# Optimization experiments

Hardware: AMD Instinct MI355X
Metric: run time of the kernel (lower is better)

The kernel has to match this reference:

```python
import jax, jax.numpy as jnp
import numpy as np

TAU = 0.5

def setup_inputs() -> dict:
    key = jax.random.key(0)
    ks = jax.random.split(key, 8)
    B_Nq, B_Ns, C, H, W = 16, 16, 512, 32, 32
    f_q = jax.random.normal(ks[0], (B_Nq, C, H, W), dtype=jnp.float32)
    f_s = jax.random.normal(ks[1], (B_Ns, C, H, W), dtype=jnp.float32)
    # depthwise 1x1 convs with groups=dim, bias=False -> per-channel scalar weights [C]
    w_cca_q = jax.random.normal(ks[2], (C,), dtype=jnp.float32)
    w_cca_k = jax.random.normal(ks[3], (C,), dtype=jnp.float32)
    w_cca_v = jax.random.normal(ks[4], (C,), dtype=jnp.float32)
    w_sca_q = jax.random.normal(ks[5], (C,), dtype=jnp.float32)
    w_sca_k = jax.random.normal(ks[6], (C,), dtype=jnp.float32)
    lam = jnp.float32(0.1)
    return {"f_q": f_q, "f_s": f_s, "w_cca_q": w_cca_q, "w_cca_k": w_cca_k,
            "w_cca_v": w_cca_v, "w_sca_q": w_sca_q, "w_sca_k": w_sca_k, "lam": lam}

def _dw(x, w):
    # depthwise 1x1 conv, no bias == per-channel scale; x: [B,C,H,W], w: [C]
    return x * w[None, :, None, None]

def reference(f_q, f_s, w_cca_q, w_cca_k, w_cca_v, w_sca_q, w_sca_k, lam):
    B_Nq, C, H, W = f_q.shape
    B_Ns = f_s.shape[0]
    P = H * W
    qc = _dw(f_q, w_cca_q).reshape(B_Nq, C, P)          # [B,C,P]
    kc_mean = _dw(f_s, w_cca_k).reshape(B_Ns, C, P).mean(axis=0)  # [C,P]
    vc_mean = _dw(f_s, w_cca_v).reshape(B_Ns, C, P).mean(axis=0)  # [C,P]
    # channel attention: [B,C,C]
    Ac = jax.nn.softmax(jnp.einsum('bcp,dp->bcd', qc, kc_mean) / P, axis=-1)
    f_cca_q = jnp.einsum('bcd,dp->bcp', Ac, vc_mean).reshape(B_Nq, C, H, W)
    qs = _dw(f_cca_q, w_sca_q).reshape(B_Nq, C, P)      # [B,C,P]
    ks_mean = _dw(f_s, w_sca_k).reshape(B_Ns, C, P).mean(axis=0)  # [C,P]
    # spatial affinity: [B,P,P]
    M = jnp.einsum('bcp,cq->bpq', qs, ks_mean) / (TAU * C)
    alpha = jax.nn.softmax(M.mean(axis=-1), axis=-1)    # [B_Nq,P]
    beta = jax.nn.softmax(M.mean(axis=-2), axis=-1)     # [B_Nq,P]
    beta_mean = jnp.broadcast_to(beta.mean(axis=0, keepdims=True), (B_Ns, P))
    Fq_out = f_q + lam * f_cca_q
    return (Fq_out, alpha, beta_mean)
```

## Files before the change

### kernel.cpp

```cpp
#include <hip/hip_runtime.h>

typedef __bf16 bf16;
typedef __bf16 bf16x4 __attribute__((ext_vector_type(4)));
typedef __bf16 bf16x8 __attribute__((ext_vector_type(8)));
typedef float f32x4 __attribute__((ext_vector_type(4)));


#define GLL16(g, l)                                                             \
    __builtin_amdgcn_global_load_lds((const __attribute__((address_space(1))) void*)(g), \
                                     (__attribute__((address_space(3))) void*)(l), 16, 0, 0)

__device__ inline float wave_reduce_sum(float v) {
#pragma unroll
    for (int m = 32; m >= 1; m >>= 1) v += __shfl_xor(v, m, 64);
    return v;
}
__device__ inline float wave_reduce_max(float v) {
#pragma unroll
    for (int m = 32; m >= 1; m >>= 1) v = fmaxf(v, __shfl_xor(v, m, 64));
    return v;
}

__global__ void k_prep(const float* __restrict__ fs, const float* __restrict__ fq,
                       float* __restrict__ fsm32, bf16* __restrict__ fsm16,
                       bf16* __restrict__ fsmT, bf16* __restrict__ fq16,
                       float* __restrict__ rmpart) {
    __shared__ bf16 tile[32][33];
    int bx = blockIdx.x, by = blockIdx.y;
    int p0 = bx * 32, c0 = by * 32;
    int t = threadIdx.x;
    int cy = t >> 3, px = (t & 7) * 4;
    size_t off = (size_t)(c0 + cy) * 1024 + p0 + px;
    float4 s = {0.f, 0.f, 0.f, 0.f};
#pragma unroll
    for (int b = 0; b < 16; ++b) {
        float4 v = *(const float4*)(fs + (size_t)b * 524288 + off);
        s.x += v.x; s.y += v.y; s.z += v.z; s.w += v.w;
    }
    s.x *= (1.f / 16.f); s.y *= (1.f / 16.f); s.z *= (1.f / 16.f); s.w *= (1.f / 16.f);
    *(float4*)(fsm32 + off) = s;
    bf16x4 h4 = {(bf16)s.x, (bf16)s.y, (bf16)s.z, (bf16)s.w};
    *(bf16x4*)(fsm16 + off) = h4;
    tile[cy][px] = h4[0];
    tile[cy][px + 1] = h4[1];
    tile[cy][px + 2] = h4[2];
    tile[cy][px + 3] = h4[3];
    float rp = s.x + s.y + s.z + s.w;
    rp += __shfl_xor(rp, 1, 64);
    rp += __shfl_xor(rp, 2, 64);
    rp += __shfl_xor(rp, 4, 64);
    if ((t & 7) == 0) rmpart[bx * 512 + c0 + cy] = rp;
    __syncthreads();
    int tx = t & 31, ty = t >> 5;
#pragma unroll
    for (int i = 0; i < 4; ++i)
        fsmT[(size_t)(p0 + ty + 8 * i) * 512 + c0 + tx] = tile[tx][ty + 8 * i];
    int blk = by * 32 + bx;
    const float4* f4 = (const float4*)fq;
#pragma unroll
    for (int i = 0; i < 16; ++i) {
        int idx = blk * 4096 + i * 256 + t;
        float4 v = f4[idx];
        bf16x4 q4 = {(bf16)v.x, (bf16)v.y, (bf16)v.z, (bf16)v.w};
        *(bf16x4*)(fq16 + (size_t)idx * 4) = q4;
    }
}

__global__ void k_gemm1(const bf16* __restrict__ A, const bf16* __restrict__ B,
                        const float* __restrict__ rmpart, const float* __restrict__ wsq,
                        const float* __restrict__ wsk, float* __restrict__ rm,
                        float* __restrict__ u, float* __restrict__ G) {
    __shared__ alignas(16) bf16 As[2][64 * 64];
    __shared__ alignas(16) bf16 Bs[2][128 * 64];
    const int dt = blockIdx.x, ct = blockIdx.y, b = blockIdx.z;
    const int t = threadIdx.x, w = t >> 6, lane = t & 63;
    const int quad = lane >> 4, r15 = lane & 15;
    const int wr = w & 1, wc = w >> 1;
    if (dt == 0 && b == 0) {
        int c = ct * 64 + (t >> 2);
        float sum = 0.f;
#pragma unroll
        for (int j = 0; j < 8; ++j) sum += rmpart[((t & 3) * 8 + j) * 512 + c];
        sum += __shfl_xor(sum, 1, 64);
        sum += __shfl_xor(sum, 2, 64);
        if ((t & 3) == 0) {
            float rmv = sum * (1.f / 1024.f);
            rm[c] = rmv;
            u[c] = wsq[c] * wsk[c] * rmv * (1.f / 256.f);
        }
    }
    const bf16* Abase = A + ((size_t)(b * 512 + ct * 64)) * 1024;
    const bf16* Bbase = B + ((size_t)(dt * 128)) * 1024;
    f32x4 acc[2][4] = {};
    auto STAGE = [&](int buf, int k0) {
#pragma unroll
        for (int i = 0; i < 2; ++i) {
            int row = i * 32 + (t >> 3);
            int gchunk = (t & 7) ^ (row & 7);
            GLL16(Abase + (size_t)row * 1024 + k0 + gchunk * 8, &As[buf][(i * 256 + t) * 8]);
        }
#pragma unroll
        for (int i = 0; i < 4; ++i) {
            int row = i * 32 + (t >> 3);
            int gchunk = (t & 7) ^ (row & 7);
            GLL16(Bbase + (size_t)row * 1024 + k0 + gchunk * 8, &Bs[buf][(i * 256 + t) * 8]);
        }
    };
    STAGE(0, 0);
    STAGE(1, 64);
    for (int s = 0; s < 16; ++s) {
        if (s < 15) asm volatile("s_waitcnt vmcnt(6)" ::: "memory");
        else        asm volatile("s_waitcnt vmcnt(0)" ::: "memory");
        __builtin_amdgcn_s_barrier();
        const int cur = s & 1;
#pragma unroll
        for (int ks = 0; ks < 2; ++ks) {
            bf16x8 af[2], bfr[4];
            const int c8 = ks * 4 + quad;
#pragma unroll
            for (int mi = 0; mi < 2; ++mi) {
                int R = wr * 32 + mi * 16 + r15;
                af[mi] = *(const bf16x8*)(&As[cur][R * 64 + ((c8 ^ (R & 7)) * 8)]);
            }
#pragma unroll
            for (int j = 0; j < 4; ++j) {
                int R = wc * 64 + j * 16 + r15;
                bfr[j] = *(const bf16x8*)(&Bs[cur][R * 64 + ((c8 ^ (R & 7)) * 8)]);
            }
#pragma unroll
            for (int mi = 0; mi < 2; ++mi)
#pragma unroll
                for (int j = 0; j < 4; ++j)
                    acc[mi][j] = __builtin_amdgcn_mfma_f32_16x16x32_bf16(af[mi], bfr[j], acc[mi][j], 0, 0, 0);
        }
        __builtin_amdgcn_s_barrier();
        if (s + 2 < 16) STAGE(cur, (s + 2) * 64);
    }
#pragma unroll
    for (int mi = 0; mi < 2; ++mi) {
        float* g = G + ((size_t)(b * 512 + ct * 64 + wr * 32 + mi * 16 + quad * 4)) * 512 +
                   dt * 128 + wc * 64 + r15;
#pragma unroll
        for (int j = 0; j < 4; ++j)
#pragma unroll
            for (int ii = 0; ii < 4; ++ii)
                g[(size_t)ii * 512 + j * 16] = acc[mi][j][ii];
    }
}

__global__ void k_softmax_ac(const float* __restrict__ G, const float* __restrict__ wq,
                             const float* __restrict__ wk, const float* __restrict__ wv,
                             const float* __restrict__ rm, bf16* __restrict__ Acw,
                             float* __restrict__ r, float* __restrict__ zbuf) {
    if (blockIdx.x < 133) zbuf[blockIdx.x * 256 + threadIdx.x] = 0.f;
    int row = blockIdx.x * 4 + (threadIdx.x >> 6);
    int lane = threadIdx.x & 63;
    int c = row & 511;
    const float* g = G + (size_t)row * 512;
    float sc = wq[c] * (1.f / 1024.f);
    float v[8];
    float mx = -3.4e38f;
#pragma unroll
    for (int j = 0; j < 8; ++j) {
        int d = lane + 64 * j;
        v[j] = g[d] * sc * wk[d];
        mx = fmaxf(mx, v[j]);
    }
    mx = wave_reduce_max(mx);
    float sum = 0.f;
#pragma unroll
    for (int j = 0; j < 8; ++j) {
        v[j] = __expf(v[j] - mx);
        sum += v[j];
    }
    sum = wave_reduce_sum(sum);
    float inv = 1.f / sum;
    bf16* o = Acw + (size_t)row * 512;
    float rsum = 0.f;
#pragma unroll
    for (int j = 0; j < 8; ++j) {
        int d = lane + 64 * j;
        float aw = v[j] * inv * wv[d];
        o[d] = (bf16)aw;
        rsum += aw * rm[d];
    }
    rsum = wave_reduce_sum(rsum);
    if (lane == 0) r[row] = rsum;
}

__global__ void k_gemm2(const bf16* __restrict__ A, const bf16* __restrict__ B,
                        const float* __restrict__ fq, const float* __restrict__ lamp,
                        const float* __restrict__ u, const float* __restrict__ r,
                        const float* __restrict__ wsq, const float* __restrict__ wsk,
                        const float* __restrict__ fsm32, float* __restrict__ out,
                        float* __restrict__ alog, float* __restrict__ blog) {
    __shared__ alignas(16) bf16 As[2][64 * 64];
    __shared__ alignas(16) bf16 Bs[2][128 * 64];
    const int pt = blockIdx.x, ct = blockIdx.y, b = blockIdx.z;
    const int t = threadIdx.x, w = t >> 6, lane = t & 63;
    const int quad = lane >> 4, r15 = lane & 15;
    const int wr = w & 1, wc = w >> 1;
    const bf16* Abase = A + ((size_t)(b * 512 + ct * 64)) * 512;
    const bf16* Bbase = B + ((size_t)(pt * 128)) * 512;
    f32x4 acc[2][4] = {};
    auto STAGE = [&](int buf, int k0) {
#pragma unroll
        for (int i = 0; i < 2; ++i) {
            int row = i * 32 + (t >> 3);
            int gchunk = (t & 7) ^ (row & 7);
            GLL16(Abase + (size_t)row * 512 + k0 + gchunk * 8, &As[buf][(i * 256 + t) * 8]);
        }
#pragma unroll
        for (int i = 0; i < 4; ++i) {
            int row = i * 32 + (t >> 3);
            int gchunk = (t & 7) ^ (row & 7);
            GLL16(Bbase + (size_t)row * 512 + k0 + gchunk * 8, &Bs[buf][(i * 256 + t) * 8]);
        }
    };
    STAGE(0, 0);
    STAGE(1, 64);
    for (int s = 0; s < 8; ++s) {
        if (s < 7) asm volatile("s_waitcnt vmcnt(6)" ::: "memory");
        else       asm volatile("s_waitcnt vmcnt(0)" ::: "memory");
        __builtin_amdgcn_s_barrier();
        const int cur = s & 1;
#pragma unroll
        for (int ks = 0; ks < 2; ++ks) {
            bf16x8 af[2], bfr[4];
            const int c8 = ks * 4 + quad;
#pragma unroll
            for (int mi = 0; mi < 2; ++mi) {
                int R = wr * 32 + mi * 16 + r15;
                af[mi] = *(const bf16x8*)(&As[cur][R * 64 + ((c8 ^ (R & 7)) * 8)]);
            }
#pragma unroll
            for (int j = 0; j < 4; ++j) {
                int R = wc * 64 + j * 16 + r15;
                bfr[j] = *(const bf16x8*)(&Bs[cur][R * 64 + ((c8 ^ (R & 7)) * 8)]);
            }
#pragma unroll
            for (int mi = 0; mi < 2; ++mi)
#pragma unroll
                for (int j = 0; j < 4; ++j)
                    acc[mi][j] = __builtin_amdgcn_mfma_f32_16x16x32_bf16(af[mi], bfr[j], acc[mi][j], 0, 0, 0);
        }
        __builtin_amdgcn_s_barrier();
        if (s + 2 < 8) STAGE(cur, (s + 2) * 64);
    }
    float lam = lamp[0];
#pragma unroll
    for (int mi = 0; mi < 2; ++mi) {
        size_t rowbase = (size_t)(b * 512 + ct * 64 + wr * 32 + mi * 16 + quad * 4);
#pragma unroll
        for (int j = 0; j < 4; ++j)
#pragma unroll
            for (int ii = 0; ii < 4; ++ii) {
                size_t idx = (rowbase + ii) * 1024 + pt * 128 + wc * 64 + j * 16 + r15;
                out[idx] = fq[idx] + lam * acc[mi][j][ii];
            }
    }
    float uv[2][4];
#pragma unroll
    for (int mi = 0; mi < 2; ++mi)
#pragma unroll
        for (int ii = 0; ii < 4; ++ii)
            uv[mi][ii] = u[ct * 64 + wr * 32 + mi * 16 + quad * 4 + ii];
#pragma unroll
    for (int j = 0; j < 4; ++j) {
        float pv = 0.f;
#pragma unroll
        for (int mi = 0; mi < 2; ++mi)
#pragma unroll
            for (int ii = 0; ii < 4; ++ii)
                pv += uv[mi][ii] * acc[mi][j][ii];
        pv += __shfl_xor(pv, 16, 64);
        pv += __shfl_xor(pv, 32, 64);
        if (lane < 16)
            atomicAdd(alog + (size_t)b * 1024 + pt * 128 + wc * 64 + j * 16 + r15, pv);
    }
    if (ct == 0) {
        __shared__ float coef[512];
        coef[t] = r[b * 512 + t] * wsq[t] * wsk[t] * (1.f / 256.f);
        coef[t + 256] = r[b * 512 + t + 256] * wsq[t + 256] * wsk[t + 256] * (1.f / 256.f);
        __syncthreads();
        int q = pt * 128 + (t & 127);
        int ch = t >> 7;
        const float* f = fsm32 + (size_t)(ch * 256) * 1024 + q;
        const float* cf = coef + ch * 256;
        float s0 = 0.f, s1 = 0.f, s2 = 0.f, s3 = 0.f;
#pragma unroll 4
        for (int ci = 0; ci < 256; ci += 4) {
            s0 += cf[ci] * f[(size_t)ci * 1024];
            s1 += cf[ci + 1] * f[(size_t)(ci + 1) * 1024];
            s2 += cf[ci + 2] * f[(size_t)(ci + 2) * 1024];
            s3 += cf[ci + 3] * f[(size_t)(ci + 3) * 1024];
        }
        atomicAdd(&blog[(size_t)b * 1024 + q], (s0 + s1) + (s2 + s3));
    }
}

__global__ void k_softmax_rows(const float* __restrict__ alog, const float* __restrict__ blog,
                               float* __restrict__ alpha_out, float* __restrict__ bmean,
                               int* __restrict__ cnt, float* __restrict__ out_bmean) {
    int z = blockIdx.x;
    int t = threadIdx.x;
    int w = t >> 6, lane = t & 63;
    const float* src = (z < 16) ? (alog + (size_t)z * 1024) : (blog + (size_t)(z - 16) * 1024);
    float v[4];
    float mx = -3.4e38f;
#pragma unroll
    for (int j = 0; j < 4; ++j) {
        v[j] = src[t + 256 * j];
        mx = fmaxf(mx, v[j]);
    }
    __shared__ float red[4];
    float wm = wave_reduce_max(mx);
    if (lane == 0) red[w] = wm;
    __syncthreads();
    mx = fmaxf(fmaxf(red[0], red[1]), fmaxf(red[2], red[3]));
    float s = 0.f;
#pragma unroll
    for (int j = 0; j < 4; ++j) {
        v[j] = __expf(v[j] - mx);
        s += v[j];
    }
    __syncthreads();
    float ws_ = wave_reduce_sum(s);
    if (lane == 0) red[w] = ws_;
    __syncthreads();
    s = red[0] + red[1] + red[2] + red[3];
    float inv = 1.f / s;
    if (z < 16) {
#pragma unroll
        for (int j = 0; j < 4; ++j) alpha_out[(size_t)z * 1024 + t + 256 * j] = v[j] * inv;
    } else {
        float inv16 = inv * (1.f / 16.f);
#pragma unroll
        for (int j = 0; j < 4; ++j) atomicAdd(&bmean[t + 256 * j], v[j] * inv16);
        __threadfence();
        __syncthreads();
        __shared__ int lastflag;
        if (t == 0) lastflag = (atomicAdd(cnt, 1) == 15) ? 1 : 0;
        __syncthreads();
        if (lastflag) {
            __threadfence();
#pragma unroll
            for (int j = 0; j < 4; ++j) {
                int q = t + 256 * j;
                float val = __hip_atomic_load(&bmean[q], __ATOMIC_ACQUIRE, __HIP_MEMORY_SCOPE_AGENT);
#pragma unroll
                for (int si = 0; si < 16; ++si) out_bmean[(size_t)si * 1024 + q] = val;
            }
        }
    }
}

extern "C" void kernel_launch(void* const* d_in, const int* in_sizes, int n_in,
                              void* d_out, int out_size, void* d_ws, size_t ws_size,
                              hipStream_t stream) {
    const float* f_q = (const float*)d_in[0];
    const float* f_s = (const float*)d_in[1];
    const float* w_cca_q = (const float*)d_in[2];
    const float* w_cca_k = (const float*)d_in[3];
    const float* w_cca_v = (const float*)d_in[4];
    const float* w_sca_q = (const float*)d_in[5];
    const float* w_sca_k = (const float*)d_in[6];
    const float* lamp = (const float*)d_in[7];

    char* ws = (char*)d_ws;
    float* fsm32 = (float*)(ws + 0);
    bf16* fsm16 = (bf16*)(ws + 2097152);
    bf16* fsmT = (bf16*)(ws + 3145728);
    float* G = (float*)(ws + 4194304);
    bf16* Acw = (bf16*)(ws + 20971520);
    bf16* fq16 = (bf16*)(ws + 29360128);
    float* rmpart = (float*)(ws + 46137344);
    float* rm = (float*)(ws + 46202880);
    float* u = (float*)(ws + 46204928);
    float* r = (float*)(ws + 46206976);
    float* alog = (float*)(ws + 46239744);
    float* blog = (float*)(ws + 46305280);
    float* bmean = (float*)(ws + 46370816);
    int* cnt = (int*)(ws + 46374912);

    float* out_fq = (float*)d_out;
    float* out_alpha = out_fq + 8388608;
    float* out_bmean = out_fq + 8404992;

    k_prep<<<dim3(32, 16), 256, 0, stream>>>(f_s, f_q, fsm32, fsm16, fsmT, fq16, rmpart);
    k_gemm1<<<dim3(4, 8, 16), 256, 0, stream>>>(fq16, fsm16, rmpart, w_sca_q, w_sca_k, rm, u, G);
    k_softmax_ac<<<2048, 256, 0, stream>>>(G, w_cca_q, w_cca_k, w_cca_v, rm, Acw, r, alog);
    k_gemm2<<<dim3(8, 8, 16), 256, 0, stream>>>(Acw, fsmT, f_q, lamp, u, r, w_sca_q, w_sca_k,
                                                fsm32, out_fq, alog, blog);
    k_softmax_rows<<<32, 256, 0, stream>>>(alog, blog, out_alpha, bmean, cnt, out_bmean);
}
```

Baseline: 172.8 us.

## Fuse five kernels into one cooperative persistent kernel with grid syncs

Replaces the five separate launches (prep, gemm1, channel softmax, gemm2, row softmax) with a single cooperative kernel of 512 blocks that runs each stage in turn, separated by grid.sync(). Stages that previously used more blocks now loop over virtual block ids. The aim is to remove per-launch overhead and inter-kernel gaps. In exchange, parallelism is capped at 512 resident blocks, gemm2 runs two tiles per block serially, the last stage uses only 32 blocks while the others idle, and every grid barrier has its own cost.

```diff
diff --git a/kernel.cpp b/kernel.cpp
--- a/kernel.cpp
+++ b/kernel.cpp
@@ -1,4 +1,7 @@
 #include <hip/hip_runtime.h>
+#include <hip/hip_cooperative_groups.h>
+
+namespace cg = cooperative_groups;
 
 typedef __bf16 bf16;
 typedef __bf16 bf16x4 __attribute__((ext_vector_type(4)));
@@ -21,335 +24,355 @@
     return v;
 }
 
-__global__ void k_prep(const float* __restrict__ fs, const float* __restrict__ fq,
-                       float* __restrict__ fsm32, bf16* __restrict__ fsm16,
-                       bf16* __restrict__ fsmT, bf16* __restrict__ fq16,
-                       float* __restrict__ rmpart) {
-    __shared__ bf16 tile[32][33];
-    int bx = blockIdx.x, by = blockIdx.y;
-    int p0 = bx * 32, c0 = by * 32;
-    int t = threadIdx.x;
-    int cy = t >> 3, px = (t & 7) * 4;
-    size_t off = (size_t)(c0 + cy) * 1024 + p0 + px;
-    float4 s = {0.f, 0.f, 0.f, 0.f};
-#pragma unroll
-    for (int b = 0; b < 16; ++b) {
-        float4 v = *(const float4*)(fs + (size_t)b * 524288 + off);
-        s.x += v.x; s.y += v.y; s.z += v.z; s.w += v.w;
+struct KParams {
+    const float* fq;
+    const float* fs;
+    const float* wq;
+    const float* wk;
+    const float* wv;
+    const float* wsq;
+    const float* wsk;
+    const float* lamp;
+    float* fsm32;
+    bf16* fsm16;
+    bf16* fsmT;
+    bf16* fq16;
+    float* rmpart;
+    float* rm;
+    float* u;
+    float* G;
+    bf16* Acw;
+    float* r;
+    float* alog;
+    float* blog;
+    float* bmean;
+    int* cnt;
+    float* out_fq;
+    float* out_alpha;
+    float* out_bmean;
+};
+
+__global__ void __launch_bounds__(256, 2) k_mega(KParams P) {
+    __shared__ __align__(16) char smem[53248];
+    cg::grid_group grid = cg::this_grid();
+    const int bid = blockIdx.x;
+    const int t = threadIdx.x;
+    const int w = t >> 6, lane = t & 63;
+    const int quad = lane >> 4, r15 = lane & 15;
+
+    {
+        bf16(*tile)[33] = (bf16(*)[33])(smem + 49152);
+        int bx = bid & 31, by = bid >> 5;
+        int p0 = bx * 32, c0 = by * 32;
+        int cy = t >> 3, px = (t & 7) * 4;
+        size_t off = (size_t)(c0 + cy) * 1024 + p0 + px;
+        float4 s = {0.f, 0.f, 0.f, 0.f};
+#pragma unroll
+        for (int b = 0; b < 16; ++b) {
+            float4 v = *(const float4*)(P.fs + (size_t)b * 524288 + off);
+            s.x += v.x; s.y += v.y; s.z += v.z; s.w += v.w;
+        }
+        s.x *= (1.f / 16.f); s.y *= (1.f / 16.f); s.z *= (1.f / 16.f); s.w *= (1.f / 16.f);
+        *(float4*)(P.fsm32 + off) = s;
+        bf16x4 h4 = {(bf16)s.x, (bf16)s.y, (bf16)s.z, (bf16)s.w};
+        *(bf16x4*)(P.fsm16 + off) = h4;
+        tile[cy][px] = h4[0];
+        tile[cy][px + 1] = h4[1];
+        tile[cy][px + 2] = h4[2];
+        tile[cy][px + 3] = h4[3];
+        float rp = s.x + s.y + s.z + s.w;
+        rp += __shfl_xor(rp, 1, 64);
+        rp += __shfl_xor(rp, 2, 64);
+        rp += __shfl_xor(rp, 4, 64);
+        if ((t & 7) == 0) P.rmpart[bx * 512 + c0 + cy] = rp;
+        __syncthreads();
+        int tx = t & 31, ty = t >> 5;
+#pragma unroll
+        for (int i = 0; i < 4; ++i)
+            P.fsmT[(size_t)(p0 + ty + 8 * i) * 512 + c0 + tx] = tile[tx][ty + 8 * i];
+        int blk = by * 32 + bx;
+        const float4* f4 = (const float4*)P.fq;
+#pragma unroll
+        for (int i = 0; i < 16; ++i) {
+            int idx = blk * 4096 + i * 256 + t;
+            float4 v = f4[idx];
+            bf16x4 q4 = {(bf16)v.x, (bf16)v.y, (bf16)v.z, (bf16)v.w};
+            *(bf16x4*)(P.fq16 + (size_t)idx * 4) = q4;
+        }
     }
-    s.x *= (1.f / 16.f); s.y *= (1.f / 16.f); s.z *= (1.f / 16.f); s.w *= (1.f / 16.f);
-    *(float4*)(fsm32 + off) = s;
-    bf16x4 h4 = {(bf16)s.x, (bf16)s.y, (bf16)s.z, (bf16)s.w};
-    *(bf16x4*)(fsm16 + off) = h4;
-    tile[cy][px] = h4[0];
-    tile[cy][px + 1] = h4[1];
-    tile[cy][px + 2] = h4[2];
-    tile[cy][px + 3] = h4[3];
-    float rp = s.x + s.y + s.z + s.w;
-    rp += __shfl_xor(rp, 1, 64);
-    rp += __shfl_xor(rp, 2, 64);
-    rp += __shfl_xor(rp, 4, 64);
-    if ((t & 7) == 0) rmpart[bx * 512 + c0 + cy] = rp;
-    __syncthreads();
-    int tx = t & 31, ty = t >> 5;
-#pragma unroll
-    for (int i = 0; i < 4; ++i)
-        fsmT[(size_t)(p0 + ty + 8 * i) * 512 + c0 + tx] = tile[tx][ty + 8 * i];
-    int blk = by * 32 + bx;
-    const float4* f4 = (const float4*)fq;
-#pragma unroll
-    for (int i = 0; i < 16; ++i) {
-        int idx = blk * 4096 + i * 256 + t;
-        float4 v = f4[idx];
-        bf16x4 q4 = {(bf16)v.x, (bf16)v.y, (bf16)v.z, (bf16)v.w};
-        *(bf16x4*)(fq16 + (size_t)idx * 4) = q4;
+    grid.sync();
+
+    {
+        bf16* As = (bf16*)smem;
+        bf16* Bs = (bf16*)(smem + 16384);
+        const int dt = bid & 3, ct = (bid >> 2) & 7, b = bid >> 5;
+        const int wr = w & 1, wc = w >> 1;
+        if (dt == 0 && b == 0) {
+            int c = ct * 64 + (t >> 2);
+            float sum = 0.f;
+#pragma unroll
+            for (int j = 0; j < 8; ++j) sum += P.rmpart[((t & 3) * 8 + j) * 512 + c];
+            sum += __shfl_xor(sum, 1, 64);
+            sum += __shfl_xor(sum, 2, 64);
+            if ((t & 3) == 0) {
+                float rmv = sum * (1.f / 1024.f);
+                P.rm[c] = rmv;
+                P.u[c] = P.wsq[c] * P.wsk[c] * rmv * (1.f / 256.f);
+            }
+        }
+        const bf16* Abase = P.fq16 + ((size_t)(b * 512 + ct * 64)) * 1024;
+        const bf16* Bbase = P.fsm16 + ((size_t)(dt * 128)) * 1024;
+        f32x4 acc[2][4] = {};
+        auto STAGE = [&](int buf, int k0) {
+#pragma unroll
+            for (int i = 0; i < 2; ++i) {
+                int row = i * 32 + (t >> 3);
+                int gchunk = (t & 7) ^ (row & 7);
+                GLL16(Abase + (size_t)row * 1024 + k0 + gchunk * 8, As + buf * 4096 + (i * 256 + t) * 8);
+            }
+#pragma unroll
+            for (int i = 0; i < 4; ++i) {
+                int row = i * 32 + (t >> 3);
+                int gchunk = (t & 7) ^ (row & 7);
+                GLL16(Bbase + (size_t)row * 1024 + k0 + gchunk * 8, Bs + buf * 8192 + (i * 256 + t) * 8);
+            }
+        };
+        STAGE(0, 0);
+        STAGE(1, 64);
+        for (int s = 0; s < 16; ++s) {
+            if (s < 15) asm volatile("s_waitcnt vmcnt(6)" ::: "memory");
+            else        asm volatile("s_waitcnt vmcnt(0)" ::: "memory");
+            __builtin_amdgcn_s_barrier();
+            const int cur = s & 1;
+#pragma unroll
+            for (int ks = 0; ks < 2; ++ks) {
+                bf16x8 af[2], bfr[4];
+                const int c8 = ks * 4 + quad;
+#pragma unroll
+                for (int mi = 0; mi < 2; ++mi) {
+                    int R = wr * 32 + mi * 16 + r15;
+                    af[mi] = *(const bf16x8*)(As + cur * 4096 + R * 64 + ((c8 ^ (R & 7)) * 8));
+                }
+#pragma unroll
+                for (int j = 0; j < 4; ++j) {
+                    int R = wc * 64 + j * 16 + r15;
+                    bfr[j] = *(const bf16x8*)(Bs + cur * 8192 + R * 64 + ((c8 ^ (R & 7)) * 8));
+                }
+#pragma unroll
+                for (int mi = 0; mi < 2; ++mi)
+#pragma unroll
+                    for (int j = 0; j < 4; ++j)
+                        acc[mi][j] = __builtin_amdgcn_mfma_f32_16x16x32_bf16(af[mi], bfr[j], acc[mi][j], 0, 0, 0);
+            }
+            __builtin_amdgcn_s_barrier();
+            if (s + 2 < 16) STAGE(cur, (s + 2) * 64);
+        }
+#pragma unroll
+        for (int mi = 0; mi < 2; ++mi) {
+            float* g = P.G + ((size_t)(b * 512 + ct * 64 + wr * 32 + mi * 16 + quad * 4)) * 512 +
+                       dt * 128 + wc * 64 + r15;
+#pragma unroll
+            for (int j = 0; j < 4; ++j)
+#pragma unroll
+                for (int ii = 0; ii < 4; ++ii)
+                    g[(size_t)ii * 512 + j * 16] = acc[mi][j][ii];
+        }
     }
-}
-
-__global__ void k_gemm1(const bf16* __restrict__ A, const bf16* __restrict__ B,
-                        const float* __restrict__ rmpart, const float* __restrict__ wsq,
-                        const float* __restrict__ wsk, float* __restrict__ rm,
-                        float* __restrict__ u, float* __restrict__ G) {
-    __shared__ alignas(16) bf16 As[2][64 * 64];
-    __shared__ alignas(16) bf16 Bs[2][128 * 64];
-    const int dt = blockIdx.x, ct = blockIdx.y, b = blockIdx.z;
-    const int t = threadIdx.x, w = t >> 6, lane = t & 63;
-    const int quad = lane >> 4, r15 = lane & 15;
-    const int wr = w & 1, wc = w >> 1;
-    if (dt == 0 && b == 0) {
-        int c = ct * 64 + (t >> 2);
+    grid.sync();
+
+    for (int v = bid; v < 2048; v += 512) {
+        if (v < 133) P.alog[v * 256 + t] = 0.f;
+        int row = v * 4 + (t >> 6);
+        int c = row & 511;
+        const float* g = P.G + (size_t)row * 512;
+        float sc = P.wq[c] * (1.f / 1024.f);
+        float vv[8];
+        float mx = -3.4e38f;
+#pragma unroll
+        for (int j = 0; j < 8; ++j) {
+            int d = lane + 64 * j;
+            vv[j] = g[d] * sc * P.wk[d];
+            mx = fmaxf(mx, vv[j]);
+        }
+        mx = wave_reduce_max(mx);
         float sum = 0.f;
 #pragma unroll
-        for (int j = 0; j < 8; ++j) sum += rmpart[((t & 3) * 8 + j) * 512 + c];
-        sum += __shfl_xor(sum, 1, 64);
-        sum += __shfl_xor(sum, 2, 64);
-        if ((t & 3) == 0) {
-            float rmv = sum * (1.f / 1024.f);
-            rm[c] = rmv;
-            u[c] = wsq[c] * wsk[c] * rmv * (1.f / 256.f);
-        }
+        for (int j = 0; j < 8; ++j) {
+            vv[j] = __expf(vv[j] - mx);
+            sum += vv[j];
+        }
+        sum = wave_reduce_sum(sum);
+        float inv = 1.f / sum;
+        bf16* o = P.Acw + (size_t)row * 512;
+        float rsum = 0.f;
+#pragma unroll
+        for (int j = 0; j < 8; ++j) {
+            int d = lane + 64 * j;
+            float aw = vv[j] * inv * P.wv[d];
+            o[d] = (bf16)aw;
+            rsum += aw * P.rm[d];
+        }
+        rsum = wave_reduce_sum(rsum);
+        if (lane == 0) P.r[row] = rsum;
     }
-    const bf16* Abase = A + ((size_t)(b * 512 + ct * 64)) * 1024;
-    const bf16* Bbase = B + ((size_t)(dt * 128)) * 1024;
-    f32x4 acc[2][4] = {};
-    auto STAGE = [&](int buf, int k0) {
-#pragma unroll
-        for (int i = 0; i < 2; ++i) {
-            int row = i * 32 + (t >> 3);
-            int gchunk = (t & 7) ^ (row & 7);
-            GLL16(Abase + (size_t)row * 1024 + k0 + gchunk * 8, &As[buf][(i * 256 + t) * 8]);
-        }
-#pragma unroll
-        for (int i = 0; i < 4; ++i) {
-            int row = i * 32 + (t >> 3);
-            int gchunk = (t & 7) ^ (row & 7);
-            GLL16(Bbase + (size_t)row * 1024 + k0 + gchunk * 8, &Bs[buf][(i * 256 + t) * 8]);
-        }
-    };
-    STAGE(0, 0);
-    STAGE(1, 64);
-    for (int s = 0; s < 16; ++s) {
-        if (s < 15) asm volatile("s_waitcnt vmcnt(6)" ::: "memory");
-        else        asm volatile("s_waitcnt vmcnt(0)" ::: "memory");
-        __builtin_amdgcn_s_barrier();
-        const int cur = s & 1;
-#pragma unroll
-        for (int ks = 0; ks < 2; ++ks) {
-            bf16x8 af[2], bfr[4];
-            const int c8 = ks * 4 + quad;
+    grid.sync();
+
+    {
+        bf16* As = (bf16*)smem;
+        bf16* Bs = (bf16*)(smem + 16384);
+        float lam = P.lamp[0];
+        for (int v = bid; v < 1024; v += 512) {
+            const int pt = v & 7, ct = (v >> 3) & 7, b = v >> 6;
+            const int wr = w & 1, wc = w >> 1;
+            const bf16* Abase = P.Acw + ((size_t)(b * 512 + ct * 64)) * 512;
+            const bf16* Bbase = P.fsmT + ((size_t)(pt * 128)) * 512;
+            f32x4 acc[2][4] = {};
+            auto STAGE = [&](int buf, int k0) {
+#pragma unroll
+                for (int i = 0; i < 2; ++i) {
+                    int row = i * 32 + (t >> 3);
+                    int gchunk = (t & 7) ^ (row & 7);
+                    GLL16(Abase + (size_t)row * 512 + k0 + gchunk * 8, As + buf * 4096 + (i * 256 + t) * 8);
+                }
+#pragma unroll
+                for (int i = 0; i < 4; ++i) {
+                    int row = i * 32 + (t >> 3);
+                    int gchunk = (t & 7) ^ (row & 7);
+                    GLL16(Bbase + (size_t)row * 512 + k0 + gchunk * 8, Bs + buf * 8192 + (i * 256 + t) * 8);
+                }
+            };
+            STAGE(0, 0);
+            STAGE(1, 64);
+            for (int s = 0; s < 8; ++s) {
+                if (s < 7) asm volatile("s_waitcnt vmcnt(6)" ::: "memory");
+                else       asm volatile("s_waitcnt vmcnt(0)" ::: "memory");
+                __builtin_amdgcn_s_barrier();
+                const int cur = s & 1;
+#pragma unroll
+                for (int ks = 0; ks < 2; ++ks) {
+                    bf16x8 af[2], bfr[4];
+                    const int c8 = ks * 4 + quad;
+#pragma unroll
+                    for (int mi = 0; mi < 2; ++mi) {
+                        int R = wr * 32 + mi * 16 + r15;
+                        af[mi] = *(const bf16x8*)(As + cur * 4096 + R * 64 + ((c8 ^ (R & 7)) * 8));
+                    }
+#pragma unroll
+                    for (int j = 0; j < 4; ++j) {
+                        int R = wc * 64 + j * 16 + r15;
+                        bfr[j] = *(const bf16x8*)(Bs + cur * 8192 + R * 64 + ((c8 ^ (R & 7)) * 8));
+                    }
+#pragma unroll
+                    for (int mi = 0; mi < 2; ++mi)
+#pragma unroll
+                        for (int j = 0; j < 4; ++j)
+                            acc[mi][j] = __builtin_amdgcn_mfma_f32_16x16x32_bf16(af[mi], bfr[j], acc[mi][j], 0, 0, 0);
+                }
+                __builtin_amdgcn_s_barrier();
+                if (s + 2 < 8) STAGE(cur, (s + 2) * 64);
+            }
 #pragma unroll
             for (int mi = 0; mi < 2; ++mi) {
-                int R = wr * 32 + mi * 16 + r15;
-                af[mi] = *(const bf16x8*)(&As[cur][R * 64 + ((c8 ^ (R & 7)) * 8)]);
-            }
+                size_t rowbase = (size_t)(b * 512 + ct * 64 + wr * 32 + mi * 16 + quad * 4);
+#pragma unroll
+                for (int j = 0; j < 4; ++j)
+#pragma unroll
+                    for (int ii = 0; ii < 4; ++ii) {
+                        size_t idx = (rowbase + ii) * 1024 + pt * 128 + wc * 64 + j * 16 + r15;
+                        P.out_fq[idx] = P.fq[idx] + lam * acc[mi][j][ii];
+                    }
+            }
+            float uv[2][4];
+#pragma unroll
+            for (int mi = 0; mi < 2; ++mi)
+#pragma unroll
+                for (int ii = 0; ii < 4; ++ii)
+                    uv[mi][ii] = P.u[ct * 64 + wr * 32 + mi * 16 + quad * 4 + ii];
 #pragma unroll
             for (int j = 0; j < 4; ++j) {
-                int R = wc * 64 + j * 16 + r15;
-                bfr[j] = *(const bf16x8*)(&Bs[cur][R * 64 + ((c8 ^ (R & 7)) * 8)]);
-            }
-#pragma unroll
-            for (int mi = 0; mi < 2; ++mi)
-#pragma unroll
-                for (int j = 0; j < 4; ++j)
-                    acc[mi][j] = __builtin_amdgcn_mfma_f32_16x16x32_bf16(af[mi], bfr[j], acc[mi][j], 0, 0, 0);
-        }
-        __builtin_amdgcn_s_barrier();
-        if (s + 2 < 16) STAGE(cur, (s + 2) * 64);
+                float pv = 0.f;
+#pragma unroll
+                for (int mi = 0; mi < 2; ++mi)
+#pragma unroll
+                    for (int ii = 0; ii < 4; ++ii)
+                        pv += uv[mi][ii] * acc[mi][j][ii];
+                pv += __shfl_xor(pv, 16, 64);
+                pv += __shfl_xor(pv, 32, 64);
+                if (lane < 16)
+                    atomicAdd(P.alog + (size_t)b * 1024 + pt * 128 + wc * 64 + j * 16 + r15, pv);
+            }
+            if (ct == 0) {
+                float* coef = (float*)(smem + 49152);
+                __syncthreads();
+                coef[t] = P.r[b * 512 + t] * P.wsq[t] * P.wsk[t] * (1.f / 256.f);
+                coef[t + 256] = P.r[b * 512 + t + 256] * P.wsq[t + 256] * P.wsk[t + 256] * (1.f / 256.f);
+                __syncthreads();
+                int q = pt * 128 + (t & 127);
+                int ch = t >> 7;
+                const float* f = P.fsm32 + (size_t)(ch * 256) * 1024 + q;
+                const float* cf = coef + ch * 256;
+                float s0 = 0.f, s1 = 0.f, s2 = 0.f, s3 = 0.f;
+#pragma unroll 4
+                for (int ci = 0; ci < 256; ci += 4) {
+                    s0 += cf[ci] * f[(size_t)ci * 1024];
+                    s1 += cf[ci + 1] * f[(size_t)(ci + 1) * 1024];
+                    s2 += cf[ci + 2] * f[(size_t)(ci + 2) * 1024];
+                    s3 += cf[ci + 3] * f[(size_t)(ci + 3) * 1024];
+                }
+                atomicAdd(&P.blog[(size_t)b * 1024 + q], (s0 + s1) + (s2 + s3));
+            }
+        }
     }
-#pragma unroll
-    for (int mi = 0; mi < 2; ++mi) {
-        float* g = G + ((size_t)(b * 512 + ct * 64 + wr * 32 + mi * 16 + quad * 4)) * 512 +
-                   dt * 128 + wc * 64 + r15;
-#pragma unroll
-        for (int j = 0; j < 4; ++j)
-#pragma unroll
-            for (int ii = 0; ii < 4; ++ii)
-                g[(size_t)ii * 512 + j * 16] = acc[mi][j][ii];
-    }
-}
-
-__global__ void k_softmax_ac(const float* __restrict__ G, const float* __restrict__ wq,
-                             const float* __restrict__ wk, const float* __restrict__ wv,
-                             const float* __restrict__ rm, bf16* __restrict__ Acw,
-                             float* __restrict__ r, float* __restrict__ zbuf) {
-    if (blockIdx.x < 133) zbuf[blockIdx.x * 256 + threadIdx.x] = 0.f;
-    int row = blockIdx.x * 4 + (threadIdx.x >> 6);
-    int lane = threadIdx.x & 63;
-    int c = row & 511;
-    const float* g = G + (size_t)row * 512;
-    float sc = wq[c] * (1.f / 1024.f);
-    float v[8];
-    float mx = -3.4e38f;
-#pragma unroll
-    for (int j = 0; j < 8; ++j) {
-        int d = lane + 64 * j;
-        v[j] = g[d] * sc * wk[d];
-        mx = fmaxf(mx, v[j]);
-    }
-    mx = wave_reduce_max(mx);
-    float sum = 0.f;
-#pragma unroll
-    for (int j = 0; j < 8; ++j) {
-        v[j] = __expf(v[j] - mx);
-        sum += v[j];
-    }
-    sum = wave_reduce_sum(sum);
-    float inv = 1.f / sum;
-    bf16* o = Acw + (size_t)row * 512;
-    float rsum = 0.f;
-#pragma unroll
-    for (int j = 0; j < 8; ++j) {
-        int d = lane + 64 * j;
-        float aw = v[j] * inv * wv[d];
-        o[d] = (bf16)aw;
-        rsum += aw * rm[d];
-    }
-    rsum = wave_reduce_sum(rsum);
-    if (lane == 0) r[row] = rsum;
-}
-
-__global__ void k_gemm2(const bf16* __restrict__ A, const bf16* __restrict__ B,
-                        const float* __restrict__ fq, const float* __restrict__ lamp,
-                        const float* __restrict__ u, const float* __restrict__ r,
-                        const float* __restrict__ wsq, const float* __restrict__ wsk,
-                        const float* __restrict__ fsm32, float* __restrict__ out,
-                        float* __restrict__ alog, float* __restrict__ blog) {
-    __shared__ alignas(16) bf16 As[2][64 * 64];
-    __shared__ alignas(16) bf16 Bs[2][128 * 64];
-    const int pt = blockIdx.x, ct = blockIdx.y, b = blockIdx.z;
-    const int t = threadIdx.x, w = t >> 6, lane = t & 63;
-    const int quad = lane >> 4, r15 = lane & 15;
-    const int wr = w & 1, wc = w >> 1;
-    const bf16* Abase = A + ((size_t)(b * 512 + ct * 64)) * 512;
-    const bf16* Bbase = B + ((size_t)(pt * 128)) * 512;
-    f32x4 acc[2][4] = {};
-    auto STAGE = [&](int buf, int k0) {
-#pragma unroll
-        for (int i = 0; i < 2; ++i) {
-            int row = i * 32 + (t >> 3);
-            int gchunk = (t & 7) ^ (row & 7);
-            GLL16(Abase + (size_t)row * 512 + k0 + gchunk * 8, &As[buf][(i * 256 + t) * 8]);
-        }
-#pragma unroll
-        for (int i = 0; i < 4; ++i) {
-            int row = i * 32 + (t >> 3);
-            int gchunk = (t & 7) ^ (row & 7);
-            GLL16(Bbase + (size_t)row * 512 + k0 + gchunk * 8, &Bs[buf][(i * 256 + t) * 8]);
-        }
-    };
-    STAGE(0, 0);
-    STAGE(1, 64);
-    for (int s = 0; s < 8; ++s) {
-        if (s < 7) asm volatile("s_waitcnt vmcnt(6)" ::: "memory");
-        else       asm volatile("s_waitcnt vmcnt(0)" ::: "memory");
-        __builtin_amdgcn_s_barrier();
-        const int cur = s & 1;
-#pragma unroll
-        for (int ks = 0; ks < 2; ++ks) {
-            bf16x8 af[2], bfr[4];
-            const int c8 = ks * 4 + quad;
-#pragma unroll
-            for (int mi = 0; mi < 2; ++mi) {
-                int R = wr * 32 + mi * 16 + r15;
-                af[mi] = *(const bf16x8*)(&As[cur][R * 64 + ((c8 ^ (R & 7)) * 8)]);
-            }
-#pragma unroll
-            for (int j = 0; j < 4; ++j) {
-                int R = wc * 64 + j * 16 + r15;
-                bfr[j] = *(const bf16x8*)(&Bs[cur][R * 64 + ((c8 ^ (R & 7)) * 8)]);
-            }
-#pragma unroll
-            for (int mi = 0; mi < 2; ++mi)
-#pragma unroll
-                for (int j = 0; j < 4; ++j)
-                    acc[mi][j] = __builtin_amdgcn_mfma_f32_16x16x32_bf16(af[mi], bfr[j], acc[mi][j], 0, 0, 0);
-        }
-        __builtin_amdgcn_s_barrier();
-        if (s + 2 < 8) STAGE(cur, (s + 2) * 64);
-    }
-    float lam = lamp[0];
-#pragma unroll
-    for (int mi = 0; mi < 2; ++mi) {
-        size_t rowbase = (size_t)(b * 512 + ct * 64 + wr * 32 + mi * 16 + quad * 4);
-#pragma unroll
-        for (int j = 0; j < 4; ++j)
-#pragma unroll
-            for (int ii = 0; ii < 4; ++ii) {
-                size_t idx = (rowbase + ii) * 1024 + pt * 128 + wc * 64 + j * 16 + r15;
-                out[idx] = fq[idx] + lam * acc[mi][j][ii];
-            }
-    }
-    float uv[2][4];
-#pragma unroll
-    for (int mi = 0; mi < 2; ++mi)
-#pragma unroll
-        for (int ii = 0; ii < 4; ++ii)
-            uv[mi][ii] = u[ct * 64 + wr * 32 + mi * 16 + quad * 4 + ii];
-#pragma unroll
-    for (int j = 0; j < 4; ++j) {
-        float pv = 0.f;
-#pragma unroll
-        for (int mi = 0; mi < 2; ++mi)
-#pragma unroll
-            for (int ii = 0; ii < 4; ++ii)
-                pv += uv[mi][ii] * acc[mi][j][ii];
-        pv += __shfl_xor(pv, 16, 64);
-        pv += __shfl_xor(pv, 32, 64);
-        if (lane < 16)
-            atomicAdd(alog + (size_t)b * 1024 + pt * 128 + wc * 64 + j * 16 + r15, pv);
-    }
-    if (ct == 0) {
-        __shared__ float coef[512];
-        coef[t] = r[b * 512 + t] * wsq[t] * wsk[t] * (1.f / 256.f);
-        coef[t + 256] = r[b * 512 + t + 256] * wsq[t + 256] * wsk[t + 256] * (1.f / 256.f);
+    grid.sync();
+
+    if (bid < 32) {
+        int z = bid;
+        float* red = (float*)(smem + 49152);
+        int* lastflag = (int*)(smem + 49152 + 64);
+        const float* src = (z < 16) ? (P.alog + (size_t)z * 1024) : (P.blog + (size_t)(z - 16) * 1024);
+        float v[4];
+        float mx = -3.4e38f;
+#pragma unroll
+        for (int j = 0; j < 4; ++j) {
+            v[j] = src[t + 256 * j];
+            mx = fmaxf(mx, v[j]);
+        }
+        float wm = wave_reduce_max(mx);
+        if (lane == 0) red[w] = wm;
         __syncthreads();
-        int q = pt * 128 + (t & 127);
-        int ch = t >> 7;
-        const float* f = fsm32 + (size_t)(ch * 256) * 1024 + q;
-        const float* cf = coef + ch * 256;
-        float s0 = 0.f, s1 = 0.f, s2 = 0.f, s3 = 0.f;
-#pragma unroll 4
-        for (int ci = 0; ci < 256; ci += 4) {
-            s0 += cf[ci] * f[(size_t)ci * 1024];
-            s1 += cf[ci + 1] * f[(size_t)(ci + 1) * 1024];
-            s2 += cf[ci + 2] * f[(size_t)(ci + 2) * 1024];
-            s3 += cf[ci + 3] * f[(size_t)(ci + 3) * 1024];
-        }
-        atomicAdd(&blog[(size_t)b * 1024 + q], (s0 + s1) + (s2 + s3));
-    }
-}
-
-__global__ void k_softmax_rows(const float* __restrict__ alog, const float* __restrict__ blog,
-                               float* __restrict__ alpha_out, float* __restrict__ bmean,
-                               int* __restrict__ cnt, float* __restrict__ out_bmean) {
-    int z = blockIdx.x;
-    int t = threadIdx.x;
-    int w = t >> 6, lane = t & 63;
-    const float* src = (z < 16) ? (alog + (size_t)z * 1024) : (blog + (size_t)(z - 16) * 1024);
-    float v[4];
-    float mx = -3.4e38f;
-#pragma unroll
-    for (int j = 0; j < 4; ++j) {
-        v[j] = src[t + 256 * j];
-        mx = fmaxf(mx, v[j]);
-    }
-    __shared__ float red[4];
-    float wm = wave_reduce_max(mx);
-    if (lane == 0) red[w] = wm;
-    __syncthreads();
-    mx = fmaxf(fmaxf(red[0], red[1]), fmaxf(red[2], red[3]));
-    float s = 0.f;
-#pragma unroll
-    for (int j = 0; j < 4; ++j) {
-        v[j] = __expf(v[j] - mx);
-        s += v[j];
-    }
-    __syncthreads();
-    float ws_ = wave_reduce_sum(s);
-    if (lane == 0) red[w] = ws_;
-    __syncthreads();
-    s = red[0] + red[1] + red[2] + red[3];
-    float inv = 1.f / s;
-    if (z < 16) {
-#pragma unroll
-        for (int j = 0; j < 4; ++j) alpha_out[(size_t)z * 1024 + t + 256 * j] = v[j] * inv;
-    } else {
-        float inv16 = inv * (1.f / 16.f);
-#pragma unroll
-        for (int j = 0; j < 4; ++j) atomicAdd(&bmean[t + 256 * j], v[j] * inv16);
-        __threadfence();
+        mx = fmaxf(fmaxf(red[0], red[1]), fmaxf(red[2], red[3]));
+        float s = 0.f;
+#pragma unroll
+        for (int j = 0; j < 4; ++j) {
+            v[j] = __expf(v[j] - mx);
+            s += v[j];
+        }
         __syncthreads();
-        __shared__ int lastflag;
-        if (t == 0) lastflag = (atomicAdd(cnt, 1) == 15) ? 1 : 0;
+        float ws_ = wave_reduce_sum(s);
+        if (lane == 0) red[w] = ws_;
         __syncthreads();
-        if (lastflag) {
+        s = red[0] + red[1] + red[2] + red[3];
+        float inv = 1.f / s;
+        if (z < 16) {
+#pragma unroll
+            for (int j = 0; j < 4; ++j) P.out_alpha[(size_t)z * 1024 + t + 256 * j] = v[j] * inv;
+        } else {
+            float inv16 = inv * (1.f / 16.f);
+#pragma unroll
+            for (int j = 0; j < 4; ++j) atomicAdd(&P.bmean[t + 256 * j], v[j] * inv16);
             __threadfence();
-#pragma unroll
-            for (int j = 0; j < 4; ++j) {
-                int q = t + 256 * j;
-                float val = __hip_atomic_load(&bmean[q], __ATOMIC_ACQUIRE, __HIP_MEMORY_SCOPE_AGENT);
-#pragma unroll
-                for (int si = 0; si < 16; ++si) out_bmean[(size_t)si * 1024 + q] = val;
+            __syncthreads();
+            if (t == 0) *lastflag = (atomicAdd(P.cnt, 1) == 15) ? 1 : 0;
+            __syncthreads();
+            if (*lastflag) {
+                __threadfence();
+#pragma unroll
+                for (int j = 0; j < 4; ++j) {
+                    int q = t + 256 * j;
+                    float val = __hip_atomic_load(&P.bmean[q], __ATOMIC_ACQUIRE, __HIP_MEMORY_SCOPE_AGENT);
+#pragma unroll
+                    for (int si = 0; si < 16; ++si) P.out_bmean[(size_t)si * 1024 + q] = val;
+                }
             }
         }
     }
@@ -358,39 +381,36 @@
 extern "C" void kernel_launch(void* const* d_in, const int* in_sizes, int n_in,
                               void* d_out, int out_size, void* d_ws, size_t ws_size,
                               hipStream_t stream) {
-    const float* f_q = (const float*)d_in[0];
-    const float* f_s = (const float*)d_in[1];
-    const float* w_cca_q = (const float*)d_in[2];
-    const float* w_cca_k = (const float*)d_in[3];
-    const float* w_cca_v = (const float*)d_in[4];
-    const float* w_sca_q = (const float*)d_in[5];
-    const float* w_sca_k = (const float*)d_in[6];
-    const float* lamp = (const float*)d_in[7];
-
     char* ws = (char*)d_ws;
-    float* fsm32 = (float*)(ws + 0);
-    bf16* fsm16 = (bf16*)(ws + 2097152);
-    bf16* fsmT = (bf16*)(ws + 3145728);
-    float* G = (float*)(ws + 4194304);
-    bf16* Acw = (bf16*)(ws + 20971520);
-    bf16* fq16 = (bf16*)(ws + 29360128);
-    float* rmpart = (float*)(ws + 46137344);
-    float* rm = (float*)(ws + 46202880);
-    float* u = (float*)(ws + 46204928);
-    float* r = (float*)(ws + 46206976);
-    float* alog = (float*)(ws + 46239744);
-    float* blog = (float*)(ws + 46305280);
-    float* bmean = (float*)(ws + 46370816);
-    int* cnt = (int*)(ws + 46374912);
+    KParams P;
+    P.fq = (const float*)d_in[0];
+    P.fs = (const float*)d_in[1];
+    P.wq = (const float*)d_in[2];
+    P.wk = (const float*)d_in[3];
+    P.wv = (const float*)d_in[4];
+    P.wsq = (const float*)d_in[5];
+    P.wsk = (const float*)d_in[6];
+    P.lamp = (const float*)d_in[7];
+    P.fsm32 = (float*)(ws + 0);
+    P.fsm16 = (bf16*)(ws + 2097152);
+    P.fsmT = (bf16*)(ws + 3145728);
+    P.G = (float*)(ws + 4194304);
+    P.Acw = (bf16*)(ws + 20971520);
+    P.fq16 = (bf16*)(ws + 29360128);
+    P.rmpart = (float*)(ws + 46137344);
+    P.rm = (float*)(ws + 46202880);
+    P.u = (float*)(ws + 46204928);
+    P.r = (float*)(ws + 46206976);
+    P.alog = (float*)(ws + 46239744);
+    P.blog = (float*)(ws + 46305280);
+    P.bmean = (float*)(ws + 46370816);
+    P.cnt = (int*)(ws + 46374912);
 
     float* out_fq = (float*)d_out;
-    float* out_alpha = out_fq + 8388608;
-    float* out_bmean = out_fq + 8404992;
-
-    k_prep<<<dim3(32, 16), 256, 0, stream>>>(f_s, f_q, fsm32, fsm16, fsmT, fq16, rmpart);
-    k_gemm1<<<dim3(4, 8, 16), 256, 0, stream>>>(fq16, fsm16, rmpart, w_sca_q, w_sca_k, rm, u, G);
-    k_softmax_ac<<<2048, 256, 0, stream>>>(G, w_cca_q, w_cca_k, w_cca_v, rm, Acw, r, alog);
-    k_gemm2<<<dim3(8, 8, 16), 256, 0, stream>>>(Acw, fsmT, f_q, lamp, u, r, w_sca_q, w_sca_k,
-                                                fsm32, out_fq, alog, blog);
-    k_softmax_rows<<<32, 256, 0, stream>>>(alog, blog, out_alpha, bmean, cnt, out_bmean);
+    P.out_fq = out_fq;
+    P.out_alpha = out_fq + 8388608;
+    P.out_bmean = out_fq + 8404992;
+
+    void* args[] = {(void*)&P};
+    hipLaunchCooperativeKernel((const void*)k_mega, dim3(512), dim3(256), args, 0, stream);
 }
```

Result: slower. 441.9 us (+155.8%).
